# Optimization experiments

Hardware: AMD Instinct MI355X
Metric: run time of the kernel (lower is better)

The kernel has to match this reference:

```python
import jax, jax.numpy as jnp
import numpy as np

N_NODES = 50000
D_FEAT = 128
HIDDEN = 256
CLASSES = 40
N_EDGES = 800000


def setup_inputs() -> dict:
    key = jax.random.key(0)
    ks = jax.random.split(key, 8)
    x = jax.random.normal(ks[0], (N_NODES, D_FEAT), dtype=jnp.float32)
    edge_index = jax.random.randint(ks[1], (2, N_EDGES), 0, N_NODES, dtype=jnp.int64)
    s1 = 1.0 / np.sqrt(D_FEAT)
    s2 = 1.0 / np.sqrt(HIDDEN)
    # PyG SAGEConv: lin_l (applied to aggregated neighbors, has bias), lin_r (root, no bias)
    Wl1 = jax.random.uniform(ks[2], (HIDDEN, D_FEAT), jnp.float32, -s1, s1)
    bl1 = jnp.zeros((HIDDEN,), jnp.float32)
    Wr1 = jax.random.uniform(ks[3], (HIDDEN, D_FEAT), jnp.float32, -s1, s1)
    Wl2 = jax.random.uniform(ks[4], (CLASSES, HIDDEN), jnp.float32, -s2, s2)
    bl2 = jnp.zeros((CLASSES,), jnp.float32)
    Wr2 = jax.random.uniform(ks[5], (CLASSES, HIDDEN), jnp.float32, -s2, s2)
    return {"x": x, "edge_index": edge_index, "Wl1": Wl1, "bl1": bl1, "Wr1": Wr1,
            "Wl2": Wl2, "bl2": bl2, "Wr2": Wr2}


def _mean_aggregate(x, src, dst, n_nodes):
    # gather source features along edges, scatter-mean into destinations
    summed = jax.ops.segment_sum(x[src], dst, num_segments=n_nodes)  # [N, d]
    counts = jax.ops.segment_sum(jnp.ones((src.shape[0],), x.dtype), dst,
                                 num_segments=n_nodes)
    return summed / jnp.maximum(counts, 1.0)[:, None]


def _sage_conv(x, src, dst, Wl, bl, Wr):
    agg = _mean_aggregate(x, src, dst, x.shape[0])
    return agg @ Wl.T + bl + x @ Wr.T


def reference(x, edge_index, Wl1, bl1, Wr1, Wl2, bl2, Wr2):
    src, dst = edge_index[0], edge_index[1]
    h = _sage_conv(x, src, dst, Wl1, bl1, Wr1)
    h = jax.nn.relu(h)
    # F.dropout(training=self.training): eval-mode inference -> identity
    h = _sage_conv(h, src, dst, Wl2, bl2, Wr2)
    return jax.nn.log_softmax(h, axis=1)
```

## Files before the change

kernel.cpp:

```cpp
#include <hip/hip_runtime.h>
#include <hip/hip_bf16.h>
#include <math.h>

#define N_NODES 50000
#define D_FEAT  128
#define HIDDEN  256
#define CLASSES 40
#define N_EDGES 800000
#define P2S 64
#define R2S 48
#define HLS 264
#define ALS 136
#define NTILES 3125
#define GRID_L 512
#define NBUCK 196
#define BCAP  5120
#define BA_BLOCKS 784
#define WCVT_BLOCKS 336

typedef unsigned int  u32;
typedef unsigned short u16;
typedef __attribute__((ext_vector_type(8))) short short8;
typedef __attribute__((ext_vector_type(4))) float floatx4;

__device__ __forceinline__ float bf_lo(u32 w) { union { u32 i; float f; } u; u.i = w << 16; return u.f; }
__device__ __forceinline__ float bf_hi(u32 w) { union { u32 i; float f; } u; u.i = w & 0xffff0000u; return u.f; }
__device__ __forceinline__ float bf1(u16 h)   { union { u32 i; float f; } u; u.i = ((u32)h) << 16; return u.f; }
__device__ __forceinline__ u16 f2bf(float f) {
  union { float f; u32 i; } u; u.f = f; u32 i = u.i;
  return (u16)((i + 0x7fffu + ((i >> 16) & 1u)) >> 16);
}
__device__ __forceinline__ u32 packbf(float a, float b) { return (u32)f2bf(a) | ((u32)f2bf(b) << 16); }

__device__ __forceinline__ bool edges_are_i64(const void* eraw) {
  const long long* p = (const long long*)eraw;
  bool ok = true;
  #pragma unroll
  for (int i = 0; i < 8; i++) {
    long long v = p[(size_t)i * 100003];
    ok = ok && (v >= 0) && (v < N_NODES);
  }
  return ok;
}

__global__ __launch_bounds__(256) void cvt_x_kernel(
    const float* __restrict__ x, u16* __restrict__ xb, int* __restrict__ bcur) {
  if (blockIdx.x < 6250) {
    int i = (blockIdx.x * 256 + threadIdx.x) * 4;
    float4 v = *(const float4*)(x + i);
    u32* o = (u32*)(xb + i);
    o[0] = packbf(v.x, v.y);
    o[1] = packbf(v.z, v.w);
  } else {
    if (threadIdx.x < NBUCK) bcur[threadIdx.x] = 0;
  }
}

__global__ __launch_bounds__(256) void bucketA_kernel(
    const void* __restrict__ eraw, int* __restrict__ bcur, u32* __restrict__ bbuf,
    const float* __restrict__ Wl1, const float* __restrict__ Wr1,
    const float* __restrict__ Wl2, const float* __restrict__ Wr2,
    u16* __restrict__ wb) {
  if (blockIdx.x >= BA_BLOCKS) {
    int i = (blockIdx.x - BA_BLOCKS) * 256 + threadIdx.x;
    if (i < 32768)      wb[i] = f2bf(Wl1[i]);
    else if (i < 65536) wb[i] = f2bf(Wr1[i - 32768]);
    else if (i < 75776) wb[i] = f2bf(Wl2[i - 65536]);
    else if (i < 86016) wb[i] = f2bf(Wr2[i - 75776]);
    return;
  }
  __shared__ int hist[NBUCK], base[NBUCK], loc[NBUCK];
  const bool i64f = edges_are_i64(eraw);
  const int t = threadIdx.x;
  for (int i = t; i < NBUCK; i += 256) { hist[i] = 0; loc[i] = 0; }
  __syncthreads();

  int sreg[4], dreg[4];
  const int e0 = blockIdx.x * 1024;
  #pragma unroll
  for (int j = 0; j < 4; j++) {
    int e = e0 + j * 256 + t;
    int ss = 0, dd = -1;
    if (e < N_EDGES) {
      if (i64f) {
        const long long* p = (const long long*)eraw;
        ss = (int)p[e]; dd = (int)p[N_EDGES + e];
      } else {
        const int* p = (const int*)eraw;
        ss = p[e]; dd = p[N_EDGES + e];
      }
      if ((u32)ss >= N_NODES || (u32)dd >= N_NODES) dd = -1;
    }
    sreg[j] = ss; dreg[j] = dd;
    if (dd >= 0) atomicAdd(&hist[dd >> 8], 1);
  }
  __syncthreads();
  for (int i = t; i < NBUCK; i += 256)
    base[i] = atomicAdd(&bcur[i], hist[i]);
  __syncthreads();
  #pragma unroll
  for (int j = 0; j < 4; j++) {
    int dd = dreg[j];
    if (dd >= 0) {
      int bk = dd >> 8;
      int pos = base[bk] + atomicAdd(&loc[bk], 1);
      if (pos < BCAP)
        bbuf[(size_t)bk * BCAP + pos] = (u32)sreg[j] | ((u32)(dd & 255) << 16);
    }
  }
}

__global__ __launch_bounds__(256) void bucketBC_kernel(
    const u32* __restrict__ bbuf, const int* __restrict__ bcur,
    int* __restrict__ offsets, int* __restrict__ csr) {
  __shared__ int cnt[256];
  __shared__ int lds[256];
  const int t = threadIdx.x;
  const int b = blockIdx.x;
  int c196 = (t < NBUCK) ? min(bcur[t], BCAP) : 0;
  lds[t] = c196;
  __syncthreads();
  #pragma unroll
  for (int d = 1; d < 256; d <<= 1) {
    int v = (t >= d) ? lds[t - d] : 0;
    __syncthreads();
    lds[t] += v;
    __syncthreads();
  }
  const int btop = (b > 0) ? lds[b - 1] : 0;
  if (b == NBUCK - 1 && t == 0) offsets[N_NODES] = lds[NBUCK - 1];
  cnt[t] = 0;
  __syncthreads();
  const int n = min(bcur[b], BCAP);
  for (int i = t; i < n; i += 256) {
    u32 e = bbuf[(size_t)b * BCAP + i];
    atomicAdd(&cnt[(e >> 16) & 255], 1);
  }
  __syncthreads();
  int c = cnt[t];
  lds[t] = c;
  __syncthreads();
  #pragma unroll
  for (int d = 1; d < 256; d <<= 1) {
    int v = (t >= d) ? lds[t - d] : 0;
    __syncthreads();
    lds[t] += v;
    __syncthreads();
  }
  const int node = b * 256 + t;
  const int off = lds[t] - c + btop;
  if (node < N_NODES) offsets[node] = off;
  cnt[t] = off;
  __syncthreads();
  for (int i = t; i < n; i += 256) {
    u32 e = bbuf[(size_t)b * BCAP + i];
    int dl = (e >> 16) & 255;
    int pos = atomicAdd(&cnt[dl], 1);
    csr[pos] = (int)(e & 0xFFFFu);
  }
}

__global__ __launch_bounds__(256) void gather1_kernel(
    const u16* __restrict__ xb, const int* __restrict__ offsets,
    const int* __restrict__ csr_src, u16* __restrict__ agg1) {
  const int node = blockIdx.x * 4 + (threadIdx.x >> 6);
  const int lane = threadIdx.x & 63;
  int b = offsets[node], e = offsets[node + 1];
  float a0 = 0.f, a1 = 0.f, b0 = 0.f, b1 = 0.f;
  float c0 = 0.f, c1 = 0.f, d0 = 0.f, d1 = 0.f;
  float e0 = 0.f, e1 = 0.f, f0 = 0.f, f1 = 0.f;
  float g0 = 0.f, g1 = 0.f, h0 = 0.f, h1 = 0.f;
  int i = b;
  for (; i + 8 <= e; i += 8) {
    int s0 = csr_src[i],     s1 = csr_src[i + 1], s2 = csr_src[i + 2], s3 = csr_src[i + 3];
    int s4 = csr_src[i + 4], s5 = csr_src[i + 5], s6 = csr_src[i + 6], s7 = csr_src[i + 7];
    u32 w0 = ((const u32*)(xb + (size_t)s0 * D_FEAT))[lane];
    u32 w1 = ((const u32*)(xb + (size_t)s1 * D_FEAT))[lane];
    u32 w2 = ((const u32*)(xb + (size_t)s2 * D_FEAT))[lane];
    u32 w3 = ((const u32*)(xb + (size_t)s3 * D_FEAT))[lane];
    u32 w4 = ((const u32*)(xb + (size_t)s4 * D_FEAT))[lane];
    u32 w5 = ((const u32*)(xb + (size_t)s5 * D_FEAT))[lane];
    u32 w6 = ((const u32*)(xb + (size_t)s6 * D_FEAT))[lane];
    u32 w7 = ((const u32*)(xb + (size_t)s7 * D_FEAT))[lane];
    a0 += bf_lo(w0); a1 += bf_hi(w0);
    b0 += bf_lo(w1); b1 += bf_hi(w1);
    c0 += bf_lo(w2); c1 += bf_hi(w2);
    d0 += bf_lo(w3); d1 += bf_hi(w3);
    e0 += bf_lo(w4); e1 += bf_hi(w4);
    f0 += bf_lo(w5); f1 += bf_hi(w5);
    g0 += bf_lo(w6); g1 += bf_hi(w6);
    h0 += bf_lo(w7); h1 += bf_hi(w7);
  }
  for (; i < e; i++) {
    int s = csr_src[i];
    u32 w = ((const u32*)(xb + (size_t)s * D_FEAT))[lane];
    a0 += bf_lo(w); a1 += bf_hi(w);
  }
  float s0 = ((a0 + b0) + (c0 + d0)) + ((e0 + f0) + (g0 + h0));
  float s1 = ((a1 + b1) + (c1 + d1)) + ((e1 + f1) + (g1 + h1));
  float inv = 1.0f / (float)max(e - b, 1);
  ((u32*)(agg1 + (size_t)node * D_FEAT))[lane] = packbf(s0 * inv, s1 * inv);
}

__global__ __launch_bounds__(256, 2) void layer_kernel(
    const u16* __restrict__ agg1, const u16* __restrict__ xb,
    const u16* __restrict__ Wl1b, const u16* __restrict__ Wr1b,
    const float* __restrict__ bl1,
    const u16* __restrict__ Wl2b, const u16* __restrict__ Wr2b,
    const float* __restrict__ bl2,
    u16* __restrict__ p2b, float* __restrict__ r2f) {
  __shared__ u16 h_lds[16 * HLS];
  __shared__ u16 a_lds[16 * ALS];
  __shared__ u16 x_lds[16 * ALS];
  const int lane = threadIdx.x & 63;
  const int wave = threadIdx.x >> 6;
  const int n15  = lane & 15;
  const int quad = lane >> 4;
  const int ko   = quad * 8;
  const int colbase = wave * 64;
  const int srow = (wave << 2) + quad;
  const int scol = n15 * 8;

  short8 Bf[8][4];
  #pragma unroll
  for (int s = 0; s < 8; s++) {
    const u16* W = (s < 4) ? Wl1b : Wr1b;
    const int kk = (s & 3) * 32;
    #pragma unroll
    for (int t = 0; t < 4; t++)
      Bf[s][t] = *(const short8*)(W + (size_t)(colbase + t * 16 + n15) * D_FEAT + ko + kk);
  }

  const int  c0   = wave;
  const bool isR0 = (c0 >= 3);
  const int  tc0  = c0 - (isR0 ? 3 : 0);
  const int  wr0  = min(tc0 * 16 + n15, CLASSES - 1);
  const u16* Wc0  = (isR0 ? Wr2b : Wl2b) + (size_t)wr0 * HIDDEN + ko;
  const bool has1 = (wave < 2);
  const int  tc1  = wave + 1;
  const int  wr1  = min(tc1 * 16 + n15, CLASSES - 1);
  const u16* Wc1  = Wr2b + (size_t)wr1 * HIDDEN + ko;

  const float bias0 = bl2[min(tc0 * 16 + n15, CLASSES - 1)];
  const float bias1 = bl2[min(tc1 * 16 + n15, CLASSES - 1)];

  for (int tile = blockIdx.x; tile < NTILES; tile += GRID_L) {
    const int m0 = tile * 16;
    {
      const size_t g = (size_t)(m0 + srow) * D_FEAT + scol;
      *(short8*)(a_lds + srow * ALS + scol) = *(const short8*)(agg1 + g);
      *(short8*)(x_lds + srow * ALS + scol) = *(const short8*)(xb + g);
    }
    __syncthreads();
    {
      floatx4 acc[4];
      #pragma unroll
      for (int t = 0; t < 4; t++) acc[t] = floatx4{0.f, 0.f, 0.f, 0.f};

      short8 a[4];
      #pragma unroll
      for (int s = 0; s < 4; s++) a[s] = *(const short8*)(a_lds + n15 * ALS + ko + s * 32);
      #pragma unroll
      for (int s = 0; s < 4; s++)
        #pragma unroll
        for (int t = 0; t < 4; t++)
          acc[t] = __builtin_amdgcn_mfma_f32_16x16x32_bf16(a[s], Bf[s][t], acc[t], 0, 0, 0);
      #pragma unroll
      for (int s = 0; s < 4; s++) a[s] = *(const short8*)(x_lds + n15 * ALS + ko + s * 32);
      #pragma unroll
      for (int s = 0; s < 4; s++)
        #pragma unroll
        for (int t = 0; t < 4; t++)
          acc[t] = __builtin_amdgcn_mfma_f32_16x16x32_bf16(a[s], Bf[4 + s][t], acc[t], 0, 0, 0);

      #pragma unroll
      for (int t = 0; t < 4; t++) {
        int col = colbase + t * 16 + n15;
        float bias = bl1[col];
        #pragma unroll
        for (int r = 0; r < 4; r++) {
          float v = acc[t][r] + bias;
          v = v > 0.f ? v : 0.f;
          h_lds[(quad * 4 + r) * HLS + col] = f2bf(v);
        }
      }
    }
    __syncthreads();
    {
      floatx4 acc0 = floatx4{0.f, 0.f, 0.f, 0.f};
      floatx4 acc1 = floatx4{0.f, 0.f, 0.f, 0.f};
      #pragma unroll
      for (int s = 0; s < 8; s++) {
        short8 a2 = *(const short8*)(&h_lds[n15 * HLS + s * 32 + ko]);
        acc0 = __builtin_amdgcn_mfma_f32_16x16x32_bf16(a2, *(const short8*)(Wc0 + s * 32), acc0, 0, 0, 0);
        if (has1)
          acc1 = __builtin_amdgcn_mfma_f32_16x16x32_bf16(a2, *(const short8*)(Wc1 + s * 32), acc1, 0, 0, 0);
      }
      {
        int col = tc0 * 16 + n15;
        #pragma unroll
        for (int r = 0; r < 4; r++) {
          int row = m0 + quad * 4 + r;
          if (isR0) r2f[(size_t)row * R2S + col] = acc0[r] + bias0;
          else      p2b[(size_t)row * P2S + col] = f2bf(acc0[r]);
        }
      }
      if (has1) {
        int col = tc1 * 16 + n15;
        #pragma unroll
        for (int r = 0; r < 4; r++) {
          int row = m0 + quad * 4 + r;
          r2f[(size_t)row * R2S + col] = acc1[r] + bias1;
        }
      }
    }
    __syncthreads();
  }
}

__global__ __launch_bounds__(256) void final_kernel(
    const u16* __restrict__ p2b, const float* __restrict__ r2f,
    const int* __restrict__ offsets, const int* __restrict__ csr_src,
    float* __restrict__ out) {
  const int node  = blockIdx.x * 4 + (threadIdx.x >> 6);
  const int lane  = threadIdx.x & 63;
  const int eslot = lane >> 5;
  const int k     = lane & 31;
  const u32* p2w  = (const u32*)p2b;
  int b = offsets[node], e = offsets[node + 1];
  float slo = 0.f, shi = 0.f;
  int i = b;
  for (; i + 16 <= e; i += 16) {
    int c[8];
    #pragma unroll
    for (int j = 0; j < 8; j++) c[j] = csr_src[i + 2 * j + eslot];
    u32 w[8];
    #pragma unroll
    for (int j = 0; j < 8; j++) w[j] = p2w[((u32)c[j] << 5) + k];
    #pragma unroll
    for (int j = 0; j < 8; j++) { slo += bf_lo(w[j]); shi += bf_hi(w[j]); }
  }
  for (; i + 2 <= e; i += 2) {
    int c = csr_src[i + eslot];
    u32 w = p2w[((u32)c << 5) + k];
    slo += bf_lo(w); shi += bf_hi(w);
  }
  if (i < e && eslot == 0) {
    int c = csr_src[i];
    u32 w = p2w[((u32)c << 5) + k];
    slo += bf_lo(w); shi += bf_hi(w);
  }
  slo += __shfl_xor(slo, 32, 64);
  shi += __shfl_xor(shi, 32, 64);
  float vlo = __shfl(slo, lane >> 1, 64);
  float vhi = __shfl(shi, lane >> 1, 64);
  float ssum = (lane & 1) ? vhi : vlo;
  float inv = 1.0f / (float)max(e - b, 1);
  const bool act = (lane < CLASSES);
  float v = act ? (ssum * inv + r2f[(size_t)node * R2S + lane]) : -INFINITY;
  float mx = v;
  #pragma unroll
  for (int d = 1; d < 64; d <<= 1) mx = fmaxf(mx, __shfl_xor(mx, d, 64));
  float ex = act ? expf(v - mx) : 0.f;
  float sum = ex;
  #pragma unroll
  for (int d = 1; d < 64; d <<= 1) sum += __shfl_xor(sum, d, 64);
  float l = mx + logf(sum);
  if (act) out[(size_t)node * CLASSES + lane] = v - l;
}

extern "C" void kernel_launch(void* const* d_in, const int* in_sizes, int n_in,
                              void* d_out, int out_size, void* d_ws, size_t ws_size,
                              hipStream_t stream) {
  const float* x   = (const float*)d_in[0];
  const void*  ei  = d_in[1];
  const float* Wl1 = (const float*)d_in[2];
  const float* bl1 = (const float*)d_in[3];
  const float* Wr1 = (const float*)d_in[4];
  const float* Wl2 = (const float*)d_in[5];
  const float* bl2 = (const float*)d_in[6];
  const float* Wr2 = (const float*)d_in[7];

  char* ws = (char*)d_ws;
  size_t off = 0;
  int* csr       = (int*)(ws + off); off += (size_t)N_EDGES * 4;
  int* offsets   = (int*)(ws + off); off += 204800;
  int* bcur      = (int*)(ws + off); off += 1024;
  u32* bbuf      = (u32*)(ws + off); off += (size_t)NBUCK * BCAP * 4;
  u16* wb        = (u16*)(ws + off); off += 172288;
  u16* xb        = (u16*)(ws + off); off += (size_t)N_NODES * D_FEAT * 2;
  u16* agg1      = (u16*)(ws + off); off += (size_t)N_NODES * D_FEAT * 2;
  u16* p2b       = (u16*)(ws + off); off += (size_t)N_NODES * P2S * 2;
  float* r2f     = (float*)(ws + off); off += (size_t)N_NODES * R2S * 4;

  u16* Wl1b = wb;
  u16* Wr1b = wb + 32768;
  u16* Wl2b = wb + 65536;
  u16* Wr2b = wb + 75776;

  cvt_x_kernel<<<6251, 256, 0, stream>>>(x, xb, bcur);
  bucketA_kernel<<<BA_BLOCKS + WCVT_BLOCKS, 256, 0, stream>>>(
      ei, bcur, bbuf, Wl1, Wr1, Wl2, Wr2, wb);
  bucketBC_kernel<<<NBUCK, 256, 0, stream>>>(bbuf, bcur, offsets, csr);
  gather1_kernel<<<N_NODES / 4, 256, 0, stream>>>(xb, offsets, csr, agg1);
  layer_kernel<<<GRID_L, 256, 0, stream>>>(agg1, xb, Wl1b, Wr1b, bl1,
                                           Wl2b, Wr2b, bl2, p2b, r2f);
  final_kernel<<<N_NODES / 4, 256, 0, stream>>>(p2b, r2f, offsets, csr, (float*)d_out);
}
```

Before: 221.6 us.

## Fuse layer-1 neighbor gather into the layer GEMM kernel

Removes the separate gather1 kernel and the agg1 global buffer. Each wave of the layer kernel now gathers and mean-aggregates neighbor features for four rows of its 16-node tile directly into LDS before the MFMA stage. This saves a launch and the write and re-read of a 12.8MB intermediate. In exchange, the latency-bound gather now runs inside a persistent grid of 512 blocks with two blocks per CU, so there is less parallelism to hide gather latency than the old grid of 12500 blocks had.

```diff
diff --git a/kernel.cpp b/kernel.cpp
--- a/kernel.cpp
+++ b/kernel.cpp
@@ -47,7 +47,7 @@
     const float* __restrict__ x, u16* __restrict__ xb, int* __restrict__ bcur) {
   if (blockIdx.x < 6250) {
     int i = (blockIdx.x * 256 + threadIdx.x) * 4;
-    float4 v = *(const float4*)(x + i);
+    floatx4 v = *(const floatx4*)(x + i);
     u32* o = (u32*)(xb + i);
     o[0] = packbf(v.x, v.y);
     o[1] = packbf(v.z, v.w);
@@ -160,50 +160,9 @@
   }
 }
 
-__global__ __launch_bounds__(256) void gather1_kernel(
+__global__ __launch_bounds__(256, 2) void layer_kernel(
     const u16* __restrict__ xb, const int* __restrict__ offsets,
-    const int* __restrict__ csr_src, u16* __restrict__ agg1) {
-  const int node = blockIdx.x * 4 + (threadIdx.x >> 6);
-  const int lane = threadIdx.x & 63;
-  int b = offsets[node], e = offsets[node + 1];
-  float a0 = 0.f, a1 = 0.f, b0 = 0.f, b1 = 0.f;
-  float c0 = 0.f, c1 = 0.f, d0 = 0.f, d1 = 0.f;
-  float e0 = 0.f, e1 = 0.f, f0 = 0.f, f1 = 0.f;
-  float g0 = 0.f, g1 = 0.f, h0 = 0.f, h1 = 0.f;
-  int i = b;
-  for (; i + 8 <= e; i += 8) {
-    int s0 = csr_src[i],     s1 = csr_src[i + 1], s2 = csr_src[i + 2], s3 = csr_src[i + 3];
-    int s4 = csr_src[i + 4], s5 = csr_src[i + 5], s6 = csr_src[i + 6], s7 = csr_src[i + 7];
-    u32 w0 = ((const u32*)(xb + (size_t)s0 * D_FEAT))[lane];
-    u32 w1 = ((const u32*)(xb + (size_t)s1 * D_FEAT))[lane];
-    u32 w2 = ((const u32*)(xb + (size_t)s2 * D_FEAT))[lane];
-    u32 w3 = ((const u32*)(xb + (size_t)s3 * D_FEAT))[lane];
-    u32 w4 = ((const u32*)(xb + (size_t)s4 * D_FEAT))[lane];
-    u32 w5 = ((const u32*)(xb + (size_t)s5 * D_FEAT))[lane];
-    u32 w6 = ((const u32*)(xb + (size_t)s6 * D_FEAT))[lane];
-    u32 w7 = ((const u32*)(xb + (size_t)s7 * D_FEAT))[lane];
-    a0 += bf_lo(w0); a1 += bf_hi(w0);
-    b0 += bf_lo(w1); b1 += bf_hi(w1);
-    c0 += bf_lo(w2); c1 += bf_hi(w2);
-    d0 += bf_lo(w3); d1 += bf_hi(w3);
-    e0 += bf_lo(w4); e1 += bf_hi(w4);
-    f0 += bf_lo(w5); f1 += bf_hi(w5);
-    g0 += bf_lo(w6); g1 += bf_hi(w6);
-    h0 += bf_lo(w7); h1 += bf_hi(w7);
-  }
-  for (; i < e; i++) {
-    int s = csr_src[i];
-    u32 w = ((const u32*)(xb + (size_t)s * D_FEAT))[lane];
-    a0 += bf_lo(w); a1 += bf_hi(w);
-  }
-  float s0 = ((a0 + b0) + (c0 + d0)) + ((e0 + f0) + (g0 + h0));
-  float s1 = ((a1 + b1) + (c1 + d1)) + ((e1 + f1) + (g1 + h1));
-  float inv = 1.0f / (float)max(e - b, 1);
-  ((u32*)(agg1 + (size_t)node * D_FEAT))[lane] = packbf(s0 * inv, s1 * inv);
-}
-
-__global__ __launch_bounds__(256, 2) void layer_kernel(
-    const u16* __restrict__ agg1, const u16* __restrict__ xb,
+    const int* __restrict__ csr,
     const u16* __restrict__ Wl1b, const u16* __restrict__ Wr1b,
     const float* __restrict__ bl1,
     const u16* __restrict__ Wl2b, const u16* __restrict__ Wr2b,
@@ -248,8 +207,46 @@
     const int m0 = tile * 16;
     {
       const size_t g = (size_t)(m0 + srow) * D_FEAT + scol;
-      *(short8*)(a_lds + srow * ALS + scol) = *(const short8*)(agg1 + g);
       *(short8*)(x_lds + srow * ALS + scol) = *(const short8*)(xb + g);
+    }
+    for (int r = 0; r < 4; r++) {
+      const int row  = (wave << 2) + r;
+      const int node = m0 + row;
+      int bo = offsets[node], e = offsets[node + 1];
+      float a0 = 0.f, a1 = 0.f, b0 = 0.f, b1 = 0.f;
+      float c0_ = 0.f, c1_ = 0.f, d0 = 0.f, d1 = 0.f;
+      float e0 = 0.f, e1 = 0.f, f0 = 0.f, f1 = 0.f;
+      float g0 = 0.f, g1 = 0.f, h0 = 0.f, h1 = 0.f;
+      int i = bo;
+      for (; i + 8 <= e; i += 8) {
+        int s0 = csr[i],     s1 = csr[i + 1], s2 = csr[i + 2], s3 = csr[i + 3];
+        int s4 = csr[i + 4], s5 = csr[i + 5], s6 = csr[i + 6], s7 = csr[i + 7];
+        u32 w0 = ((const u32*)(xb + (size_t)s0 * D_FEAT))[lane];
+        u32 w1 = ((const u32*)(xb + (size_t)s1 * D_FEAT))[lane];
+        u32 w2 = ((const u32*)(xb + (size_t)s2 * D_FEAT))[lane];
+        u32 w3 = ((const u32*)(xb + (size_t)s3 * D_FEAT))[lane];
+        u32 w4 = ((const u32*)(xb + (size_t)s4 * D_FEAT))[lane];
+        u32 w5 = ((const u32*)(xb + (size_t)s5 * D_FEAT))[lane];
+        u32 w6 = ((const u32*)(xb + (size_t)s6 * D_FEAT))[lane];
+        u32 w7 = ((const u32*)(xb + (size_t)s7 * D_FEAT))[lane];
+        a0 += bf_lo(w0); a1 += bf_hi(w0);
+        b0 += bf_lo(w1); b1 += bf_hi(w1);
+        c0_ += bf_lo(w2); c1_ += bf_hi(w2);
+        d0 += bf_lo(w3); d1 += bf_hi(w3);
+        e0 += bf_lo(w4); e1 += bf_hi(w4);
+        f0 += bf_lo(w5); f1 += bf_hi(w5);
+        g0 += bf_lo(w6); g1 += bf_hi(w6);
+        h0 += bf_lo(w7); h1 += bf_hi(w7);
+      }
+      for (; i < e; i++) {
+        int s = csr[i];
+        u32 w = ((const u32*)(xb + (size_t)s * D_FEAT))[lane];
+        a0 += bf_lo(w); a1 += bf_hi(w);
+      }
+      float s0 = ((a0 + b0) + (c0_ + d0)) + ((e0 + f0) + (g0 + h0));
+      float s1 = ((a1 + b1) + (c1_ + d1)) + ((e1 + f1) + (g1 + h1));
+      float inv = 1.0f / (float)max(e - bo, 1);
+      ((u32*)(a_lds + row * ALS))[lane] = packbf(s0 * inv, s1 * inv);
     }
     __syncthreads();
     {
@@ -389,7 +386,6 @@
   u32* bbuf      = (u32*)(ws + off); off += (size_t)NBUCK * BCAP * 4;
   u16* wb        = (u16*)(ws + off); off += 172288;
   u16* xb        = (u16*)(ws + off); off += (size_t)N_NODES * D_FEAT * 2;
-  u16* agg1      = (u16*)(ws + off); off += (size_t)N_NODES * D_FEAT * 2;
   u16* p2b       = (u16*)(ws + off); off += (size_t)N_NODES * P2S * 2;
   float* r2f     = (float*)(ws + off); off += (size_t)N_NODES * R2S * 4;
 
@@ -402,8 +398,7 @@
   bucketA_kernel<<<BA_BLOCKS + WCVT_BLOCKS, 256, 0, stream>>>(
       ei, bcur, bbuf, Wl1, Wr1, Wl2, Wr2, wb);
   bucketBC_kernel<<<NBUCK, 256, 0, stream>>>(bbuf, bcur, offsets, csr);
-  gather1_kernel<<<N_NODES / 4, 256, 0, stream>>>(xb, offsets, csr, agg1);
-  layer_kernel<<<GRID_L, 256, 0, stream>>>(agg1, xb, Wl1b, Wr1b, bl1,
+  layer_kernel<<<GRID_L, 256, 0, stream>>>(xb, offsets, csr, Wl1b, Wr1b, bl1,
                                            Wl2b, Wr2b, bl2, p2b, r2f);
   final_kernel<<<N_NODES / 4, 256, 0, stream>>>(p2b, r2f, offsets, csr, (float*)d_out);
 }
```

After: 279.1 us. +25.9%, slower.
